# Kernel tuning notes

Measured on AMD Instinct MI355X. Metric: run time of the kernel, lower is better.

## Reference

```python
import jax, jax.numpy as jnp
from jax import lax
import numpy as np

PAD = 0
V, DW, H, T, B = 30000, 512, 512, 50, 128


def _xavier(key, shape):
    fan_in, fan_out = shape[1], shape[0]
    lim = float(np.sqrt(6.0 / (fan_in + fan_out)))
    return jax.random.uniform(key, shape, jnp.float32, -lim, lim)


def setup_inputs() -> dict:
    key = jax.random.key(0)
    ks = jax.random.split(key, 8)
    return {
        "user": jax.random.randint(ks[0], (B,), 0, 10000),
        "item": jax.random.randint(ks[1], (B,), 0, 10000),
        "review_input": jax.random.randint(ks[2], (T, B), 0, V),
        "review_target": jax.random.randint(ks[3], (T, B), 0, V),
        "word_emb": jax.random.normal(ks[4], (V, DW), jnp.float32) * 0.02,
        "W_ih": _xavier(ks[5], (3 * H, DW)),
        "W_hh": _xavier(ks[6], (3 * H, H)),
        "b_ih": jnp.zeros((3 * H,), jnp.float32),
        "b_hh": jnp.zeros((3 * H,), jnp.float32),
        "W_out": _xavier(ks[7], (V, H)),
        "b_out": jnp.zeros((V,), jnp.float32),
    }


def reference(user, item, review_input, review_target,
              word_emb, W_ih, W_hh, b_ih, b_hh, W_out, b_out):
    n_batch = user.shape[0]
    # embed all timesteps at once: [T, B, DW]
    x = word_emb[review_input]
    # precompute input-to-gate projections: [T, B, 3H]
    xg = jnp.einsum('tbd,gd->tbg', x, W_ih) + b_ih
    h0 = jnp.zeros((n_batch, H), x.dtype)

    def step(h, xg_t):
        hg = h @ W_hh.T + b_hh                      # [B, 3H]
        xr, xz, xn = jnp.split(xg_t, 3, axis=-1)    # PyTorch order: r, z, n
        hr, hz, hn = jnp.split(hg, 3, axis=-1)
        r = jax.nn.sigmoid(xr + hr)
        z = jax.nn.sigmoid(xz + hz)
        n = jnp.tanh(xn + r * hn)
        h_new = (1.0 - z) * n + z * h
        return h_new, h_new

    _, outs = lax.scan(step, h0, xg)                # [T, B, H]
    logits = outs.reshape(-1, H) @ W_out.T + b_out  # [T*B, V]
    tgt = review_target.reshape(-1)
    logp = jax.nn.log_softmax(logits, axis=-1)
    nll = -jnp.take_along_axis(logp, tgt[:, None], axis=1)[:, 0]
    mask = tgt != PAD
    out_loss = jnp.where(mask, nll, 0.0)            # F.cross_entropy reduction='none', ignore_index=PAD
    denom = jnp.maximum(jnp.sum(mask), 1).astype(out_loss.dtype)
    obj = jnp.sum(out_loss) / denom                 # mean over non-ignored tokens
    return out_loss, obj
```

## Files before the change

### kernel.cpp

```cpp
#include <hip/hip_runtime.h>

typedef short short8 __attribute__((ext_vector_type(8)));
typedef float f32x4 __attribute__((ext_vector_type(4)));
typedef float f4 __attribute__((ext_vector_type(4)));
typedef unsigned short ushort_t;

#define VOCAB 30000
#define DW 512
#define KDIM 512
#define HDIM 512
#define G3 1536
#define TT 50
#define BB 128
#define M_ROWS 6400
#define NPAD 30208
#define NT2 472

__device__ __forceinline__ float b2f(ushort_t u){ return __uint_as_float(((unsigned)u)<<16); }
__device__ __forceinline__ ushort_t f2b(float f){
    unsigned u = __float_as_uint(f);
    unsigned r = (u + 0x7fffu + ((u>>16)&1u)) >> 16;
    return (ushort_t)r;
}
__device__ __forceinline__ float sigf(float x){
    float e = __expf(-x);
    return __builtin_amdgcn_rcpf(1.0f + e);
}
__device__ __forceinline__ float tanh_(float x){
    return 2.0f*sigf(2.0f*x) - 1.0f;
}
__device__ __forceinline__ void gload16(const ushort_t* g, char* l){
    __builtin_amdgcn_global_load_lds((const __attribute__((address_space(1))) void*)g,
                                     (__attribute__((address_space(3))) void*)l, 16, 0, 0);
}

__global__ void k_setup(const f4* __restrict__ s, ushort_t* __restrict__ d,
                        const f4* __restrict__ wih, const f4* __restrict__ whh,
                        ushort_t* __restrict__ dih, ushort_t* __restrict__ dhh,
                        const float* __restrict__ bi, const float* __restrict__ bh,
                        float* __restrict__ bg, float* __restrict__ hf,
                        ushort_t* __restrict__ hb){
    int i = blockIdx.x*blockDim.x + threadIdx.x;
    uint2 o = make_uint2(0u, 0u);
    if (i < VOCAB*DW/4){
        f4 v = s[i];
        o.x = (unsigned)f2b(v[0]) | ((unsigned)f2b(v[1]) << 16);
        o.y = (unsigned)f2b(v[2]) | ((unsigned)f2b(v[3]) << 16);
    }
    *(uint2*)(d + (size_t)i*4) = o;
    if (i < G3*DW/4){
        f4 v = wih[i];
        unsigned lo = (unsigned)f2b(v[0]) | ((unsigned)f2b(v[1]) << 16);
        unsigned hi = (unsigned)f2b(v[2]) | ((unsigned)f2b(v[3]) << 16);
        *(uint2*)(dih + (size_t)i*4) = make_uint2(lo, hi);
        v = whh[i];
        lo = (unsigned)f2b(v[0]) | ((unsigned)f2b(v[1]) << 16);
        hi = (unsigned)f2b(v[2]) | ((unsigned)f2b(v[3]) << 16);
        *(uint2*)(dhh + (size_t)i*4) = make_uint2(lo, hi);
        if (i < G3) bg[i] = bi[i] + (i < 2*HDIM ? bh[i] : 0.0f);
        if (i < BB*HDIM){ hf[i] = 0.0f; hb[i] = 0; }
    }
}
__global__ void k_gather(const float* __restrict__ emb, const int* __restrict__ idx,
                         ushort_t* __restrict__ x){
    int row = blockIdx.x;
    int v = idx[row];
    const float2* src = (const float2*)(emb + (size_t)v*DW);
    unsigned* dst = (unsigned*)(x + (size_t)row*DW);
    for (int d = threadIdx.x; d < DW/2; d += blockDim.x){
        float2 w = src[d];
        dst[d] = (unsigned)f2b(w.x) | ((unsigned)f2b(w.y) << 16);
    }
}

template<int NBLK>
__global__ __launch_bounds__(256, 3) void k_gemmA(const ushort_t* __restrict__ A,
        const ushort_t* __restrict__ Bw, const float* __restrict__ bias,
        ushort_t* __restrict__ Cout){
    __shared__ ushort_t As[128*32];
    __shared__ ushort_t Bs[128*32];
    const int nwg = NBLK * 50;
    const int q = nwg >> 3;
    int wgid = (blockIdx.x & 7)*q + (blockIdx.x >> 3);
    int band = wgid / (10*NBLK);
    int rr   = wgid % (10*NBLK);
    int nb = rr / 10;
    int mb = band*10 + (rr % 10);
    int n0 = nb*128, m0 = mb*128;

    int lane = threadIdx.x & 63, wv = threadIdx.x >> 6;
    int lo = lane & 15, hi = lane >> 4;
    int wr = wv >> 1, wc = wv & 1;
    f32x4 acc[4][4] = {};
    int xsl = ((lane & 3) ^ ((lane >> 3) & 3)) * 8;
    const ushort_t* gA = A  + (size_t)(m0 + wv*32 + (lane>>2))*KDIM + xsl;
    const ushort_t* gB = Bw + (size_t)(n0 + wv*32 + (lane>>2))*KDIM + xsl;
    char* lA = (char*)As + wv*2048;
    char* lB = (char*)Bs + wv*2048;
    int rchunk = (hi ^ ((lo >> 1) & 3)) * 8;
    for (int kt = 0; kt < 16; ++kt){
        __syncthreads();
        int k0 = kt*32;
        gload16(gA + k0,           lA);
        gload16(gA + 16*KDIM + k0, lA + 1024);
        gload16(gB + k0,           lB);
        gload16(gB + 16*KDIM + k0, lB + 1024);
        __syncthreads();
        short8 av[4], bv[4];
        #pragma unroll
        for (int mi = 0; mi < 4; ++mi)
            av[mi] = *(const short8*)&As[(wr*64 + mi*16 + lo)*32 + rchunk];
        #pragma unroll
        for (int ni = 0; ni < 4; ++ni)
            bv[ni] = *(const short8*)&Bs[(wc*64 + ni*16 + lo)*32 + rchunk];
        #pragma unroll
        for (int mi = 0; mi < 4; ++mi)
            #pragma unroll
            for (int ni = 0; ni < 4; ++ni)
                acc[mi][ni] = __builtin_amdgcn_mfma_f32_16x16x32_bf16(av[mi], bv[ni], acc[mi][ni], 0, 0, 0);
    }
    #pragma unroll
    for (int ni = 0; ni < 4; ++ni){
        int n = n0 + wc*64 + ni*16 + lo;
        float bb = bias[n];
        #pragma unroll
        for (int mi = 0; mi < 4; ++mi){
            #pragma unroll
            for (int j = 0; j < 4; ++j){
                int m = m0 + wr*64 + mi*16 + hi*4 + j;
                Cout[(size_t)m*G3 + n] = f2b(acc[mi][ni][j] + bb);
            }
        }
    }
}

template<int NBLK>
__global__ __launch_bounds__(256, 4) void k_gemmC(const ushort_t* __restrict__ A,
        const ushort_t* __restrict__ Bw, const float* __restrict__ bo,
        float* __restrict__ psum){
    __shared__ ushort_t As[128*64];
    __shared__ ushort_t Bs[128*64];
    const int nwg = NBLK * 50;
    const int q = nwg >> 3;
    int wgid = (blockIdx.x & 7)*q + (blockIdx.x >> 3);
    int band = wgid / (10*NBLK);
    int rr   = wgid % (10*NBLK);
    int nb = rr / 10;
    int mb = band*10 + (rr % 10);
    int n0 = nb*128, m0 = mb*128;

    int tid = threadIdx.x;
    int lane = tid & 63, wv = tid >> 6;
    int lo = lane & 15, hi = lane >> 4;
    int wr = wv >> 1, wc = wv & 1;
    f32x4 acc[4][4] = {};
    int srow = lane >> 3;
    int xslot = (lane & 7) ^ srow;
    const ushort_t* gA = A  + (size_t)(m0 + wv*32 + srow)*KDIM + xslot*8;
    const ushort_t* gB = Bw + (size_t)(n0 + wv*32 + srow)*KDIM + xslot*8;
    char* lA = (char*)As + (size_t)(wv*32)*128;
    char* lB = (char*)Bs + (size_t)(wv*32)*128;
    for (int kt = 0; kt < 8; ++kt){
        __syncthreads();
        int k0 = kt*64;
        #pragma unroll
        for (int c4 = 0; c4 < 4; ++c4){
            gload16(gA + (size_t)c4*8*KDIM + k0, lA + c4*8*128);
            gload16(gB + (size_t)c4*8*KDIM + k0, lB + c4*8*128);
        }
        __syncthreads();
        short8 av[4][2], bv[4][2];
        #pragma unroll
        for (int mi = 0; mi < 4; ++mi){
            int rrow = wr*64 + mi*16 + lo;
            #pragma unroll
            for (int ks = 0; ks < 2; ++ks)
                av[mi][ks] = *(const short8*)&As[rrow*64 + (((ks*4+hi) ^ (lo&7)))*8];
        }
        #pragma unroll
        for (int ni = 0; ni < 4; ++ni){
            int rrow = wc*64 + ni*16 + lo;
            #pragma unroll
            for (int ks = 0; ks < 2; ++ks)
                bv[ni][ks] = *(const short8*)&Bs[rrow*64 + (((ks*4+hi) ^ (lo&7)))*8];
        }
        #pragma unroll
        for (int mi = 0; mi < 4; ++mi)
            #pragma unroll
            for (int ni = 0; ni < 4; ++ni){
                acc[mi][ni] = __builtin_amdgcn_mfma_f32_16x16x32_bf16(av[mi][0], bv[ni][0], acc[mi][ni], 0, 0, 0);
                acc[mi][ni] = __builtin_amdgcn_mfma_f32_16x16x32_bf16(av[mi][1], bv[ni][1], acc[mi][ni], 0, 0, 0);
            }
    }
    float bov[4];
    bool valid[4];
    #pragma unroll
    for (int ni = 0; ni < 4; ++ni){
        int col = n0 + wc*64 + ni*16 + lo;
        valid[ni] = (col < VOCAB);
        bov[ni] = valid[ni] ? bo[col] : 0.0f;
    }
    int tile = nb*2 + wc;
    #pragma unroll
    for (int mi = 0; mi < 4; ++mi){
        #pragma unroll
        for (int j = 0; j < 4; ++j){
            float s = 0.0f;
            #pragma unroll
            for (int ni = 0; ni < 4; ++ni)
                s += valid[ni] ? __expf(acc[mi][ni][j] + bov[ni]) : 0.0f;
            for (int d = 1; d < 16; d <<= 1) s += __shfl_xor(s, d, 64);
            if (lo == 0){
                int m = m0 + wr*64 + mi*16 + hi*4 + j;
                psum[(size_t)m*NT2 + tile] = s;
            }
        }
    }
}

__global__ __launch_bounds__(256) void k_step(const ushort_t* __restrict__ hprev_b,
        const float* __restrict__ hprev_f, const ushort_t* __restrict__ Whh,
        const ushort_t* __restrict__ xg, const float* __restrict__ bh,
        float* __restrict__ hnext_f, ushort_t* __restrict__ hnext_b,
        ushort_t* __restrict__ outs, int t){
    __shared__ float gl[3][4][16][17];
    int tid = threadIdx.x;
    int lane = tid & 63, wv = tid >> 6;
    int lo = lane & 15, hi = lane >> 4;
    int c16 = blockIdx.x * 16;
    int b0  = blockIdx.y * 16;
    f32x4 acc[3] = {};
    const ushort_t* Arow = hprev_b + (size_t)(b0 + lo)*HDIM + wv*128;
    const ushort_t* Bbase = Whh + (size_t)(c16 + lo)*HDIM + wv*128;
    #pragma unroll
    for (int kk = 0; kk < 4; ++kk){
        int k0 = kk*32 + hi*8;
        short8 a = *(const short8*)(Arow + k0);
        #pragma unroll
        for (int g = 0; g < 3; ++g){
            short8 b = *(const short8*)(Bbase + (size_t)g*HDIM*HDIM + k0);
            acc[g] = __builtin_amdgcn_mfma_f32_16x16x32_bf16(a, b, acc[g], 0, 0, 0);
        }
    }
    #pragma unroll
    for (int g = 0; g < 3; ++g)
        #pragma unroll
        for (int j = 0; j < 4; ++j)
            gl[g][wv][hi*4 + j][lo] = acc[g][j];
    __syncthreads();
    int b = tid >> 4, c = tid & 15;
    int bt = b0 + b, cc = c16 + c;
    float hr = gl[0][0][b][c] + gl[0][1][b][c] + gl[0][2][b][c] + gl[0][3][b][c];
    float hz = gl[1][0][b][c] + gl[1][1][b][c] + gl[1][2][b][c] + gl[1][3][b][c];
    float hn = gl[2][0][b][c] + gl[2][1][b][c] + gl[2][2][b][c] + gl[2][3][b][c];
    const ushort_t* xgt = xg + (size_t)t*BB*G3 + (size_t)bt*G3;
    float xr = b2f(xgt[cc]);
    float xz = b2f(xgt[HDIM + cc]);
    float xn = b2f(xgt[2*HDIM + cc]);
    float r  = sigf(hr + xr);
    float z  = sigf(hz + xz);
    float n  = tanh_(xn + r*(hn + bh[2*HDIM + cc]));
    float hold = hprev_f[(size_t)bt*HDIM + cc];
    float hnew = (1.0f - z)*n + z*hold;
    hnext_f[(size_t)bt*HDIM + cc] = hnew;
    ushort_t hv = f2b(hnew);
    hnext_b[(size_t)bt*HDIM + cc] = hv;
    outs[((size_t)t*BB + bt)*HDIM + cc] = hv;
}

__global__ __launch_bounds__(256) void k_loss(const ushort_t* __restrict__ outs,
        const ushort_t* __restrict__ Wo, const float* __restrict__ bo,
        const float* __restrict__ psum, const int* __restrict__ tgt,
        float* __restrict__ out){
    int lane = threadIdx.x & 63, wv = threadIdx.x >> 6;
    int row = blockIdx.x*4 + wv;
    int tg = tgt[row];
    const float* ps = psum + (size_t)row*NT2;
    float S = 0.0f;
    for (int t = lane; t < NT2; t += 64) S += ps[t];
    for (int d = 1; d < 64; d <<= 1) S += __shfl_xor(S, d, 64);
    float lse = __logf(S);
    const ushort_t* a = outs + (size_t)row*HDIM + lane*8;
    const ushort_t* w = Wo + (size_t)tg*DW + lane*8;
    float s = 0.0f;
    #pragma unroll
    for (int j = 0; j < 8; ++j) s += b2f(a[j]) * b2f(w[j]);
    for (int d = 1; d < 64; d <<= 1) s += __shfl_xor(s, d, 64);
    if (lane == 0){
        float logit = s + bo[tg];
        out[row] = (tg != 0) ? (lse - logit) : 0.0f;
    }
}

__global__ __launch_bounds__(1024) void k_obj(const float* __restrict__ loss,
        const int* __restrict__ tgt, float* __restrict__ out){
    __shared__ float ss[1024];
    __shared__ int   sc[1024];
    float s = 0.0f; int c = 0;
    for (int i = threadIdx.x; i < M_ROWS; i += 1024){
        s += loss[i];
        c += (tgt[i] != 0) ? 1 : 0;
    }
    ss[threadIdx.x] = s; sc[threadIdx.x] = c;
    __syncthreads();
    for (int d = 512; d > 0; d >>= 1){
        if (threadIdx.x < (unsigned)d){ ss[threadIdx.x] += ss[threadIdx.x+d]; sc[threadIdx.x] += sc[threadIdx.x+d]; }
        __syncthreads();
    }
    if (threadIdx.x == 0) out[M_ROWS] = ss[0] / (float)(sc[0] > 0 ? sc[0] : 1);
}

extern "C" void kernel_launch(void* const* d_in, const int* in_sizes, int n_in,
                              void* d_out, int out_size, void* d_ws, size_t ws_size,
                              hipStream_t stream) {
    const int*   review_input  = (const int*)d_in[2];
    const int*   review_target = (const int*)d_in[3];
    const float* word_emb = (const float*)d_in[4];
    const float* W_ih = (const float*)d_in[5];
    const float* W_hh = (const float*)d_in[6];
    const float* b_ih = (const float*)d_in[7];
    const float* b_hh = (const float*)d_in[8];
    const float* W_out = (const float*)d_in[9];
    const float* b_out = (const float*)d_in[10];
    float* out = (float*)d_out;
    (void)n_in; (void)in_sizes; (void)out_size; (void)ws_size;

    char* ws = (char*)d_ws;
    size_t off = 0;
    auto alloc = [&](size_t bytes)->char*{
        char* p = ws + off;
        off = (off + bytes + 255) & ~(size_t)255;
        return p;
    };
    ushort_t* Wout_b = (ushort_t*)alloc((size_t)NPAD*DW*2);
    ushort_t* Wih_b  = (ushort_t*)alloc((size_t)G3*DW*2);
    ushort_t* Whh_b  = (ushort_t*)alloc((size_t)G3*HDIM*2);
    ushort_t* outs_b = (ushort_t*)alloc((size_t)M_ROWS*HDIM*2);
    float*    biasg  = (float*)alloc((size_t)G3*4);
    float*    h_f    = (float*)alloc((size_t)2*BB*HDIM*4);
    ushort_t* h_b    = (ushort_t*)alloc((size_t)2*BB*HDIM*2);
    ushort_t* xb     = (ushort_t*)alloc((size_t)M_ROWS*DW*2);
    ushort_t* xg     = (ushort_t*)alloc((size_t)M_ROWS*G3*2);
    float*    psum   = (float*)xb;

    k_setup<<<NPAD*DW/4/256, 256, 0, stream>>>((const f4*)W_out, Wout_b,
                                               (const f4*)W_ih, (const f4*)W_hh,
                                               Wih_b, Whh_b, b_ih, b_hh, biasg, h_f, h_b);
    k_gather<<<M_ROWS, 256, 0, stream>>>(word_emb, review_input, xb);

    k_gemmA<12><<<600, 256, 0, stream>>>(xb, Wih_b, biasg, xg);

    for (int t = 0; t < TT; ++t){
        int cur = t & 1, nxt = cur ^ 1;
        k_step<<<dim3(HDIM/16, BB/16), 256, 0, stream>>>(h_b + (size_t)cur*BB*HDIM,
                                       h_f + (size_t)cur*BB*HDIM,
                                       Whh_b, xg, b_hh,
                                       h_f + (size_t)nxt*BB*HDIM,
                                       h_b + (size_t)nxt*BB*HDIM,
                                       outs_b, t);
    }

    k_gemmC<236><<<11800, 256, 0, stream>>>(outs_b, Wout_b, b_out, psum);
    k_loss<<<M_ROWS/4, 256, 0, stream>>>(outs_b, Wout_b, b_out, psum, review_target, out);
    k_obj<<<1, 1024, 0, stream>>>(out, review_target, out);
}
```

Baseline: 488.9 us.

## Fuse gather into setup, widen gemmA K-tile, single-wave GRU step

The embedding gather moves into the setup kernel, which removes one launch. The input-projection GEMM now loads 64-wide K tiles with an 8-slot XOR swizzle, which halves the number of sync rounds at the cost of more LDS per block. The recurrent step kernel drops from four waves with an LDS reduction to one wave that loops over the full K and applies the gates straight from the MFMA accumulators. This removes shared memory and barriers from the 50 serial steps but gives each step less parallelism.

Result: no change. 483.5 us (-1.1%).

```diff
diff --git a/kernel.cpp b/kernel.cpp
--- a/kernel.cpp
+++ b/kernel.cpp
@@ -39,7 +39,9 @@
                         ushort_t* __restrict__ dih, ushort_t* __restrict__ dhh,
                         const float* __restrict__ bi, const float* __restrict__ bh,
                         float* __restrict__ bg, float* __restrict__ hf,
-                        ushort_t* __restrict__ hb){
+                        ushort_t* __restrict__ hb,
+                        const float* __restrict__ emb, const int* __restrict__ idx,
+                        ushort_t* __restrict__ xb){
     int i = blockIdx.x*blockDim.x + threadIdx.x;
     uint2 o = make_uint2(0u, 0u);
     if (i < VOCAB*DW/4){
@@ -60,25 +62,21 @@
         if (i < G3) bg[i] = bi[i] + (i < 2*HDIM ? bh[i] : 0.0f);
         if (i < BB*HDIM){ hf[i] = 0.0f; hb[i] = 0; }
     }
-}
-__global__ void k_gather(const float* __restrict__ emb, const int* __restrict__ idx,
-                         ushort_t* __restrict__ x){
-    int row = blockIdx.x;
-    int v = idx[row];
-    const float2* src = (const float2*)(emb + (size_t)v*DW);
-    unsigned* dst = (unsigned*)(x + (size_t)row*DW);
-    for (int d = threadIdx.x; d < DW/2; d += blockDim.x){
-        float2 w = src[d];
-        dst[d] = (unsigned)f2b(w.x) | ((unsigned)f2b(w.y) << 16);
+    if (blockIdx.x < M_ROWS){
+        int row = blockIdx.x;
+        int v = idx[row];
+        float2 w = ((const float2*)(emb + (size_t)v*DW))[threadIdx.x];
+        ((unsigned*)(xb + (size_t)row*DW))[threadIdx.x] =
+            (unsigned)f2b(w.x) | ((unsigned)f2b(w.y) << 16);
     }
 }
 
 template<int NBLK>
-__global__ __launch_bounds__(256, 3) void k_gemmA(const ushort_t* __restrict__ A,
+__global__ __launch_bounds__(256, 4) void k_gemmA(const ushort_t* __restrict__ A,
         const ushort_t* __restrict__ Bw, const float* __restrict__ bias,
         ushort_t* __restrict__ Cout){
-    __shared__ ushort_t As[128*32];
-    __shared__ ushort_t Bs[128*32];
+    __shared__ ushort_t As[128*64];
+    __shared__ ushort_t Bs[128*64];
     const int nwg = NBLK * 50;
     const int q = nwg >> 3;
     int wgid = (blockIdx.x & 7)*q + (blockIdx.x >> 3);
@@ -88,36 +86,48 @@
     int mb = band*10 + (rr % 10);
     int n0 = nb*128, m0 = mb*128;
 
-    int lane = threadIdx.x & 63, wv = threadIdx.x >> 6;
+    int tid = threadIdx.x;
+    int lane = tid & 63, wv = tid >> 6;
     int lo = lane & 15, hi = lane >> 4;
     int wr = wv >> 1, wc = wv & 1;
     f32x4 acc[4][4] = {};
-    int xsl = ((lane & 3) ^ ((lane >> 3) & 3)) * 8;
-    const ushort_t* gA = A  + (size_t)(m0 + wv*32 + (lane>>2))*KDIM + xsl;
-    const ushort_t* gB = Bw + (size_t)(n0 + wv*32 + (lane>>2))*KDIM + xsl;
-    char* lA = (char*)As + wv*2048;
-    char* lB = (char*)Bs + wv*2048;
-    int rchunk = (hi ^ ((lo >> 1) & 3)) * 8;
-    for (int kt = 0; kt < 16; ++kt){
-        __syncthreads();
-        int k0 = kt*32;
-        gload16(gA + k0,           lA);
-        gload16(gA + 16*KDIM + k0, lA + 1024);
-        gload16(gB + k0,           lB);
-        gload16(gB + 16*KDIM + k0, lB + 1024);
-        __syncthreads();
-        short8 av[4], bv[4];
+    int srow = lane >> 3;
+    int xslot = (lane & 7) ^ srow;
+    const ushort_t* gA = A  + (size_t)(m0 + wv*32 + srow)*KDIM + xslot*8;
+    const ushort_t* gB = Bw + (size_t)(n0 + wv*32 + srow)*KDIM + xslot*8;
+    char* lA = (char*)As + (size_t)(wv*32)*128;
+    char* lB = (char*)Bs + (size_t)(wv*32)*128;
+    for (int kt = 0; kt < 8; ++kt){
+        __syncthreads();
+        int k0 = kt*64;
+        #pragma unroll
+        for (int c4 = 0; c4 < 4; ++c4){
+            gload16(gA + (size_t)c4*8*KDIM + k0, lA + c4*8*128);
+            gload16(gB + (size_t)c4*8*KDIM + k0, lB + c4*8*128);
+        }
+        __syncthreads();
+        short8 av[4][2], bv[4][2];
+        #pragma unroll
+        for (int mi = 0; mi < 4; ++mi){
+            int rrow = wr*64 + mi*16 + lo;
+            #pragma unroll
+            for (int ks = 0; ks < 2; ++ks)
+                av[mi][ks] = *(const short8*)&As[rrow*64 + (((ks*4+hi) ^ (lo&7)))*8];
+        }
+        #pragma unroll
+        for (int ni = 0; ni < 4; ++ni){
+            int rrow = wc*64 + ni*16 + lo;
+            #pragma unroll
+            for (int ks = 0; ks < 2; ++ks)
+                bv[ni][ks] = *(const short8*)&Bs[rrow*64 + (((ks*4+hi) ^ (lo&7)))*8];
+        }
         #pragma unroll
         for (int mi = 0; mi < 4; ++mi)
-            av[mi] = *(const short8*)&As[(wr*64 + mi*16 + lo)*32 + rchunk];
-        #pragma unroll
-        for (int ni = 0; ni < 4; ++ni)
-            bv[ni] = *(const short8*)&Bs[(wc*64 + ni*16 + lo)*32 + rchunk];
-        #pragma unroll
-        for (int mi = 0; mi < 4; ++mi)
-            #pragma unroll
-            for (int ni = 0; ni < 4; ++ni)
-                acc[mi][ni] = __builtin_amdgcn_mfma_f32_16x16x32_bf16(av[mi], bv[ni], acc[mi][ni], 0, 0, 0);
+            #pragma unroll
+            for (int ni = 0; ni < 4; ++ni){
+                acc[mi][ni] = __builtin_amdgcn_mfma_f32_16x16x32_bf16(av[mi][0], bv[ni][0], acc[mi][ni], 0, 0, 0);
+                acc[mi][ni] = __builtin_amdgcn_mfma_f32_16x16x32_bf16(av[mi][1], bv[ni][1], acc[mi][ni], 0, 0, 0);
+            }
     }
     #pragma unroll
     for (int ni = 0; ni < 4; ++ni){
@@ -218,54 +228,46 @@
     }
 }
 
-__global__ __launch_bounds__(256) void k_step(const ushort_t* __restrict__ hprev_b,
+__global__ __launch_bounds__(64) void k_step(const ushort_t* __restrict__ hprev_b,
         const float* __restrict__ hprev_f, const ushort_t* __restrict__ Whh,
         const ushort_t* __restrict__ xg, const float* __restrict__ bh,
         float* __restrict__ hnext_f, ushort_t* __restrict__ hnext_b,
         ushort_t* __restrict__ outs, int t){
-    __shared__ float gl[3][4][16][17];
-    int tid = threadIdx.x;
-    int lane = tid & 63, wv = tid >> 6;
+    int lane = threadIdx.x;
     int lo = lane & 15, hi = lane >> 4;
     int c16 = blockIdx.x * 16;
     int b0  = blockIdx.y * 16;
     f32x4 acc[3] = {};
-    const ushort_t* Arow = hprev_b + (size_t)(b0 + lo)*HDIM + wv*128;
-    const ushort_t* Bbase = Whh + (size_t)(c16 + lo)*HDIM + wv*128;
-    #pragma unroll
-    for (int kk = 0; kk < 4; ++kk){
+    const ushort_t* Arow = hprev_b + (size_t)(b0 + lo)*HDIM;
+    #pragma unroll
+    for (int kk = 0; kk < 16; ++kk){
         int k0 = kk*32 + hi*8;
         short8 a = *(const short8*)(Arow + k0);
         #pragma unroll
         for (int g = 0; g < 3; ++g){
-            short8 b = *(const short8*)(Bbase + (size_t)g*HDIM*HDIM + k0);
+            short8 b = *(const short8*)(Whh + (size_t)(g*HDIM + c16 + lo)*HDIM + k0);
             acc[g] = __builtin_amdgcn_mfma_f32_16x16x32_bf16(a, b, acc[g], 0, 0, 0);
         }
     }
-    #pragma unroll
-    for (int g = 0; g < 3; ++g)
-        #pragma unroll
-        for (int j = 0; j < 4; ++j)
-            gl[g][wv][hi*4 + j][lo] = acc[g][j];
-    __syncthreads();
-    int b = tid >> 4, c = tid & 15;
-    int bt = b0 + b, cc = c16 + c;
-    float hr = gl[0][0][b][c] + gl[0][1][b][c] + gl[0][2][b][c] + gl[0][3][b][c];
-    float hz = gl[1][0][b][c] + gl[1][1][b][c] + gl[1][2][b][c] + gl[1][3][b][c];
-    float hn = gl[2][0][b][c] + gl[2][1][b][c] + gl[2][2][b][c] + gl[2][3][b][c];
-    const ushort_t* xgt = xg + (size_t)t*BB*G3 + (size_t)bt*G3;
-    float xr = b2f(xgt[cc]);
-    float xz = b2f(xgt[HDIM + cc]);
-    float xn = b2f(xgt[2*HDIM + cc]);
-    float r  = sigf(hr + xr);
-    float z  = sigf(hz + xz);
-    float n  = tanh_(xn + r*(hn + bh[2*HDIM + cc]));
-    float hold = hprev_f[(size_t)bt*HDIM + cc];
-    float hnew = (1.0f - z)*n + z*hold;
-    hnext_f[(size_t)bt*HDIM + cc] = hnew;
-    ushort_t hv = f2b(hnew);
-    hnext_b[(size_t)bt*HDIM + cc] = hv;
-    outs[((size_t)t*BB + bt)*HDIM + cc] = hv;
+    int c = c16 + lo;
+    float bhn = bh[2*HDIM + c];
+    const ushort_t* xgt = xg + (size_t)t*BB*G3;
+    #pragma unroll
+    for (int j = 0; j < 4; ++j){
+        int bt = b0 + hi*4 + j;
+        float xr = b2f(xgt[(size_t)bt*G3 + c]);
+        float xz = b2f(xgt[(size_t)bt*G3 + HDIM + c]);
+        float xn = b2f(xgt[(size_t)bt*G3 + 2*HDIM + c]);
+        float r  = sigf(acc[0][j] + xr);
+        float z  = sigf(acc[1][j] + xz);
+        float n  = tanh_(xn + r*(acc[2][j] + bhn));
+        float hold = hprev_f[(size_t)bt*HDIM + c];
+        float hnew = (1.0f - z)*n + z*hold;
+        hnext_f[(size_t)bt*HDIM + c] = hnew;
+        ushort_t hb = f2b(hnew);
+        hnext_b[(size_t)bt*HDIM + c] = hb;
+        outs[((size_t)t*BB + bt)*HDIM + c] = hb;
+    }
 }
 
 __global__ __launch_bounds__(256) void k_loss(const ushort_t* __restrict__ outs,
@@ -345,14 +347,14 @@
 
     k_setup<<<NPAD*DW/4/256, 256, 0, stream>>>((const f4*)W_out, Wout_b,
                                                (const f4*)W_ih, (const f4*)W_hh,
-                                               Wih_b, Whh_b, b_ih, b_hh, biasg, h_f, h_b);
-    k_gather<<<M_ROWS, 256, 0, stream>>>(word_emb, review_input, xb);
+                                               Wih_b, Whh_b, b_ih, b_hh, biasg, h_f, h_b,
+                                               word_emb, review_input, xb);
 
     k_gemmA<12><<<600, 256, 0, stream>>>(xb, Wih_b, biasg, xg);
 
     for (int t = 0; t < TT; ++t){
         int cur = t & 1, nxt = cur ^ 1;
-        k_step<<<dim3(HDIM/16, BB/16), 256, 0, stream>>>(h_b + (size_t)cur*BB*HDIM,
+        k_step<<<dim3(HDIM/16, BB/16), 64, 0, stream>>>(h_b + (size_t)cur*BB*HDIM,
                                        h_f + (size_t)cur*BB*HDIM,
                                        Whh_b, xg, b_hh,
                                        h_f + (size_t)nxt*BB*HDIM,
```
